# Performance work log

Hardware: AMD Instinct MI355X
Metric: run time of the kernel (lower is better)

## Reference

```python
import jax, jax.numpy as jnp
import numpy as np

B, T, D, H, L, W = 32, 512, 256, 8, 2, 10
NQ = 10000
HD = D // H


def setup_inputs():
    key = jax.random.key(0)
    ks = jax.random.split(key, 16)
    def n(k, shape, s=0.02):
        return jax.random.normal(k, shape, jnp.float32) * s
    return {
        "q": jax.random.randint(ks[0], (B, T), 0, NQ),
        "s": jax.random.randint(ks[1], (B, T), 0, 2),
        "q_embed": n(ks[2], (NQ + 1, D)),
        "s_embed": n(ks[3], (2, D)),
        "pos_embed": n(ks[4], (512, D)),
        "fusion_w": n(ks[5], (2 * D, D)),
        "fusion_b": jnp.zeros((D,), jnp.float32),
        "in_proj_w": n(ks[6], (L, D, 3 * D)),
        "in_proj_b": jnp.zeros((L, 3 * D), jnp.float32),
        "out_proj_w": n(ks[7], (L, D, D)),
        "out_proj_b": jnp.zeros((L, D), jnp.float32),
        "ln1_g": jnp.ones((L, D), jnp.float32),
        "ln1_b": jnp.zeros((L, D), jnp.float32),
        "ln2_g": jnp.ones((L, D), jnp.float32),
        "ln2_b": jnp.zeros((L, D), jnp.float32),
        "ff1_w": n(ks[8], (L, D, 4 * D)),
        "ff1_b": jnp.zeros((L, 4 * D), jnp.float32),
        "ff2_w": n(ks[9], (L, 4 * D, D)),
        "ff2_b": jnp.zeros((L, D), jnp.float32),
        "sw1": n(ks[10], (6, 32), 0.1),
        "sb1": jnp.zeros((32,), jnp.float32),
        "sw2": n(ks[11], (32, D // 4), 0.1),
        "sb2": jnp.zeros((D // 4,), jnp.float32),
        "cw1": n(ks[12], (D + D // 4, D)),
        "cb1": jnp.zeros((D,), jnp.float32),
        "cw2": n(ks[13], (D, 1)),
        "cb2": jnp.zeros((1,), jnp.float32),
    }


def _ln(x, g, b):
    mu = jnp.mean(x, -1, keepdims=True)
    var = jnp.mean(jnp.square(x - mu), -1, keepdims=True)
    return (x - mu) * jax.lax.rsqrt(var + 1e-5) * g + b


def _sliding_sum(x, w):
    # sum over trailing window of size w ending at each t, via prefix sums
    c = jnp.concatenate([jnp.zeros((x.shape[0], 1), x.dtype), jnp.cumsum(x, axis=1)], axis=1)
    t = jnp.arange(x.shape[1])
    return c[:, t + 1] - c[:, jnp.maximum(t + 1 - w, 0)]


def _stats(s, mask):
    # vectorized version of _extract_statistics (prefix-sum sliding windows)
    mf = mask.astype(jnp.float32)
    sf = s.astype(jnp.float32) * mf
    valid = _sliding_sum(mf, W)
    correct_rate = _sliding_sum(sf, W) / (valid + 1e-6)
    rc = _sliding_sum(mf, 5)
    recent_correct = _sliding_sum(sf, 5) / (rc + 1e-6)
    trans = ((s[:, 1:] != s[:, :-1]) & mask[:, 1:] & mask[:, :-1]).astype(jnp.float32)
    diff = jnp.concatenate([jnp.zeros((s.shape[0], 1), jnp.float32), trans], axis=1)
    change_rate = _sliding_sum(diff, W - 1) / (valid + 1e-6)
    # max consecutive equal run within each trailing window of size W
    sp = jnp.pad(s, ((0, 0), (W - 1, 0)))
    mp = jnp.pad(mask, ((0, 0), (W - 1, 0)))
    win_s = [sp[:, j:j + T] for j in range(W)]
    win_m = [mp[:, j:j + T] for j in range(W)]
    run = win_m[0].astype(jnp.float32)
    mx = run
    for j in range(1, W):  # fixed small window, not a data-dim loop
        eq = (win_s[j] == win_s[j - 1]) & win_m[j - 1]
        run = win_m[j].astype(jnp.float32) * (jnp.where(eq, run, 0.0) + 1.0)
        mx = jnp.maximum(mx, run)
    rel = jnp.broadcast_to(jnp.arange(T, dtype=jnp.float32) / max(T, 100), s.shape)
    cov = valid / W
    return jnp.stack([correct_rate, recent_correct, change_rate, mx / W, rel, cov], axis=-1)


def reference(q, s, q_embed, s_embed, pos_embed, fusion_w, fusion_b, in_proj_w, in_proj_b,
              out_proj_w, out_proj_b, ln1_g, ln1_b, ln2_g, ln2_b, ff1_w, ff1_b, ff2_w, ff2_b,
              sw1, sb1, sw2, sb2, cw1, cb1, cw2, cb2):
    mask = s >= 0
    qm = jnp.where(mask, q, 0)
    sm = jnp.where(mask, s, 0)
    h = jnp.concatenate([q_embed[qm], s_embed[sm]], axis=-1)  # [B,T,2D]
    h = jax.nn.relu(h @ fusion_w + fusion_b) + pos_embed[:T][None]
    causal = jnp.tril(jnp.ones((T, T), bool))
    allowed = causal[None, None] & mask[:, None, None, :]
    scale = 1.0 / (HD ** 0.5)
    for l in range(L):
        qkv = h @ in_proj_w[l] + in_proj_b[l]
        qh, kh, vh = jnp.split(qkv, 3, axis=-1)
        qh = qh.reshape(B, T, H, HD).transpose(0, 2, 1, 3)
        kh = kh.reshape(B, T, H, HD).transpose(0, 2, 1, 3)
        vh = vh.reshape(B, T, H, HD).transpose(0, 2, 1, 3)
        scores = jnp.einsum('bhqd,bhkd->bhqk', qh, kh) * scale
        scores = jnp.where(allowed, scores, -1e9)
        attn = jax.nn.softmax(scores, axis=-1)
        o = jnp.einsum('bhqk,bhkd->bhqd', attn, vh).transpose(0, 2, 1, 3).reshape(B, T, D)
        h = _ln(h + (o @ out_proj_w[l] + out_proj_b[l]), ln1_g[l], ln1_b[l])
        ff = jax.nn.gelu(h @ ff1_w[l] + ff1_b[l], approximate=False) @ ff2_w[l] + ff2_b[l]
        h = _ln(h + ff, ln2_g[l], ln2_b[l])
    sfeat = _stats(sm, mask)  # [B,T,6]
    semb = jax.nn.relu(sfeat @ sw1 + sb1) @ sw2 + sb2  # [B,T,D//4]
    comb = jnp.concatenate([h, semb], axis=-1)
    logits = (jax.nn.relu(comb @ cw1 + cb1) @ cw2 + cb2)[..., 0]
    return jnp.where(mask, logits, -1e9)
```

## Files before the change

kernel.cpp:

```cpp
#include <hip/hip_runtime.h>
#include <hip/hip_bf16.h>
#include <cmath>


using short8 = __attribute__((ext_vector_type(8))) short;
using short4v = __attribute__((ext_vector_type(4))) short;
using f32x4  = __attribute__((ext_vector_type(4))) float;

__device__ inline float gelu_f(float x) {
    return 0.5f * x * (1.0f + erff(x * 0.70710678118654752f));
}

__device__ inline short f2bf(float x) {
    union { float f; unsigned u; } v; v.f = x;
    return (short)((v.u + 0x7fffu + ((v.u >> 16) & 1u)) >> 16);
}

__device__ inline float bf2f(short v) {
    union { unsigned u; float f; } x; x.u = ((unsigned)(unsigned short)v) << 16;
    return x.f;
}

__device__ inline unsigned packbf(float lo, float hi) {
    union { float f; unsigned u; } a, b; a.f = lo; b.f = hi;
    unsigned ra = (a.u + 0x7fffu + ((a.u >> 16) & 1u)) >> 16;
    unsigned rb = (b.u + 0x7fffu + ((b.u >> 16) & 1u)) >> 16;
    return (rb << 16) | (ra & 0xffffu);
}

#define GLOAD16(gp, lp) __builtin_amdgcn_global_load_lds( \
    (const __attribute__((address_space(1))) void*)(gp), \
    (__attribute__((address_space(3))) void*)(lp), 16, 0, 0)

__global__ __launch_bounds__(256) void prep_kernel(
    const float* __restrict__ fusion_w, const float* __restrict__ in_proj_w,
    const float* __restrict__ out_proj_w, const float* __restrict__ ff1_w,
    const float* __restrict__ ff2_w, const float* __restrict__ cw1,
    short* __restrict__ wts,
    const int* __restrict__ q, const int* __restrict__ s,
    const float* __restrict__ qe, const float* __restrict__ se,
    short* __restrict__ A)
{
    __shared__ float tile[32][33];
    if (blockIdx.x < 1744) {
        const int b0[10]      = {0,128,320,512,576,640,896,1152,1408,1664};
        const int Ks[10]      = {512,256,256,256,256,256,256,1024,1024,320};
        const int Ns[10]      = {256,768,768,256,256,1024,1024,256,256,256};
        const int sidx[10]    = {0,1,1,2,2,3,3,4,4,5};
        const size_t soff[10] = {0,0,196608,0,65536,0,262144,0,262144,0};
        const size_t doff[10] = {0,131072,327680,524288,589824,655360,917504,1179648,1441792,1703936};
        const float* srcs[6] = {fusion_w, in_proj_w, out_proj_w, ff1_w, ff2_w, cw1};
        int bid = blockIdx.x;
        int mi = 0;
        while (mi < 9 && bid >= b0[mi + 1]) ++mi;
        int bl = bid - b0[mi];
        int K = Ks[mi], N = Ns[mi];
        int tx = bl % (N >> 5), ty = bl / (N >> 5);
        const float* src = srcs[sidx[mi]] + soff[mi];
        short* dst = wts + doff[mi];
        int c = threadIdx.x & 31, r = threadIdx.x >> 5;
#pragma unroll
        for (int i = 0; i < 4; ++i)
            tile[r + i * 8][c] = src[(size_t)(ty * 32 + r + i * 8) * N + tx * 32 + c];
        __syncthreads();
#pragma unroll
        for (int i = 0; i < 4; ++i)
            dst[(size_t)(tx * 32 + r + i * 8) * K + ty * 32 + c] = f2bf(tile[c][r + i * 8]);
    } else {
        int e8 = (blockIdx.x - 1744) * 256 + threadIdx.x;
        int row = e8 >> 6;
        int k8 = (e8 & 63) << 3;
        int sv = s[row];
        bool mk = sv >= 0;
        const float* src = (k8 < 256) ? qe + (size_t)(mk ? q[row] : 0) * 256 + k8
                                      : se + (size_t)(mk ? sv : 0) * 256 + (k8 - 256);
        float4 v0 = *(const float4*)src;
        float4 v1 = *(const float4*)(src + 4);
        short8 o;
        o[0] = f2bf(v0.x); o[1] = f2bf(v0.y); o[2] = f2bf(v0.z); o[3] = f2bf(v0.w);
        o[4] = f2bf(v1.x); o[5] = f2bf(v1.y); o[6] = f2bf(v1.z); o[7] = f2bf(v1.w);
        *(short8*)(A + (size_t)row * 512 + k8) = o;
    }
}

template<int EPI, int BN, int K>
__global__ __launch_bounds__(512) void gemm_bstat(
    const short* __restrict__ A, const short* __restrict__ Wt,
    const float* __restrict__ bias, short* __restrict__ out0,
    short* __restrict__ ok, short* __restrict__ ov,
    const float* __restrict__ pos)
{
    constexpr int SPR = K / 8;
    constexpr int NSTEP = K / 32;
    constexpr int NJ = BN / 16;
    __shared__ short Bs[BN * K];
    const int tid = threadIdx.x, lane = tid & 63, wv = tid >> 6;
    const int lg = lane >> 4, lr = lane & 15;
    const int n0 = blockIdx.y * BN;
    const int row0 = blockIdx.x * 128 + wv * 16;

#pragma unroll
    for (int i = 0; i < (BN * K) / 4096; ++i) {
        int slot = i * 512 + tid;
        int n = slot / SPR, posn = slot % SPR;
        int g = posn ^ (n & 7);
        GLOAD16(Wt + (size_t)(n0 + n) * K + g * 8, &Bs[slot * 8]);
    }
    const short* arow = A + (size_t)(row0 + lr) * K;
    short8 af[NSTEP];
#pragma unroll
    for (int kk = 0; kk < NSTEP; ++kk)
        af[kk] = *(const short8*)(arow + kk * 32 + lg * 8);
    __syncthreads();

    f32x4 acc[NJ] = {};
#pragma unroll
    for (int kk = 0; kk < NSTEP; ++kk) {
#pragma unroll
        for (int j = 0; j < NJ; ++j) {
            int n = j * 16 + lr;
            short8 b = *(const short8*)&Bs[n * K + (((kk * 4 + lg) ^ (n & 7)) << 3)];
            acc[j] = __builtin_amdgcn_mfma_f32_16x16x32_bf16(af[kk], b, acc[j], 0, 0, 0);
        }
    }

    if constexpr (EPI == 0) {
#pragma unroll
        for (int j = 0; j < NJ; ++j)
#pragma unroll
        for (int r = 0; r < 4; ++r) {
            int row = row0 + lg * 4 + r;
            int col = n0 + j * 16 + lr;
            float x = acc[j][r] + bias[col];
            x = fmaxf(x, 0.f) + pos[(size_t)(row & 511) * 256 + col];
            out0[(size_t)row * 256 + col] = f2bf(x);
        }
    } else if constexpr (EPI == 1) {
#pragma unroll
        for (int j = 0; j < NJ; ++j)
#pragma unroll
        for (int r = 0; r < 4; ++r) {
            int row = row0 + lg * 4 + r;
            int gcol = n0 + j * 16 + lr;
            int t = row & 511, bg = row >> 9;
            int sec = gcol >> 8, cc = gcol & 255;
            int h = cc >> 5, d = cc & 31, bh = bg * 8 + h;
            short v = f2bf(acc[j][r] + bias[gcol]);
            if (sec == 0)      out0[((size_t)bh * 512 + t) * 32 + d] = v;
            else if (sec == 1) ok[((size_t)bh * 512 + t) * 32 + d] = v;
            else {
                int kl = t & 31;
                ov[(size_t)bh * 16384 + (size_t)(t >> 5) * 1024 +
                   (size_t)((kl >> 2) & 3) * 256 + d * 8 + (((kl & 3) << 1) | ((kl >> 4) & 1))] = v;
            }
        }
    } else {
#pragma unroll
        for (int j = 0; j < NJ; ++j)
#pragma unroll
        for (int r = 0; r < 4; ++r) {
            int row = row0 + lg * 4 + r;
            int gcol = n0 + j * 16 + lr;
            float x = acc[j][r] + bias[gcol];
            out0[(size_t)row * 1024 + gcol] = f2bf(gelu_f(x));
        }
    }
}

template<int EPI>
__global__ __launch_bounds__(512) void gemm_red(
    const short* __restrict__ A, const short* __restrict__ A2,
    const short* __restrict__ Wt, const float* __restrict__ bias,
    short* __restrict__ hb,
    const float* __restrict__ gamma, const float* __restrict__ beta,
    const float* __restrict__ cw2, const float* __restrict__ cb2,
    const int* __restrict__ smask, float* __restrict__ outlog, int K)
{
    const int tid = threadIdx.x, lane = tid & 63, wv = tid >> 6;
    const int lg = lane >> 4, lr = lane & 15;
    const int wr = wv >> 2, wc = wv & 3;
    const int m0 = blockIdx.x * 64;

    __shared__ short As[2][2048];
    __shared__ short Bs[2][8192];
    __shared__ float redS[64][4];
    __shared__ float redQ[64][4];

    f32x4 acc[2][4] = {};
    const int nsteps = K >> 5;

    auto stage = [&](int buf, int step) {
        int k0 = step << 5;
        if (tid < 256) {
            int k = k0 + wv * 8;
            const short* srcA;
            if constexpr (EPI == 4)
                srcA = (k < 256) ? A + (size_t)(m0 + lane) * 256 + k
                                 : A2 + (size_t)(m0 + lane) * 64 + (k - 256);
            else
                srcA = A + (size_t)(m0 + lane) * K + k;
            GLOAD16(srcA, &As[buf][(wv * 64) * 8]);
        }
        {
            GLOAD16(Wt + (size_t)(tid & 255) * K + k0 + (tid >> 8) * 8,
                    &Bs[buf][(wv * 64) * 8]);
        }
        {
            int slot = tid + 512;
            GLOAD16(Wt + (size_t)(slot & 255) * K + k0 + (slot >> 8) * 8,
                    &Bs[buf][((wv + 8) * 64) * 8]);
        }
    };

    stage(0, 0);
    __syncthreads();
    for (int step = 0; step < nsteps; ++step) {
        int cur = step & 1;
        if (step + 1 < nsteps) stage(cur ^ 1, step + 1);
        short8 a[2], b[4];
#pragma unroll
        for (int i = 0; i < 2; ++i)
            a[i] = *(const short8*)&As[cur][(lg * 64 + wr * 32 + i * 16 + lr) * 8];
#pragma unroll
        for (int j = 0; j < 4; ++j)
            b[j] = *(const short8*)&Bs[cur][(lg * 256 + wc * 64 + j * 16 + lr) * 8];
#pragma unroll
        for (int i = 0; i < 2; ++i)
#pragma unroll
            for (int j = 0; j < 4; ++j)
                acc[i][j] = __builtin_amdgcn_mfma_f32_16x16x32_bf16(a[i], b[j], acc[i][j], 0, 0, 0);
        __syncthreads();
    }

    if constexpr (EPI == 3) {
        float ps[2][4], pq[2][4];
#pragma unroll
        for (int i = 0; i < 2; ++i)
#pragma unroll
        for (int r = 0; r < 4; ++r) { ps[i][r] = 0.f; pq[i][r] = 0.f; }
#pragma unroll
        for (int i = 0; i < 2; ++i)
#pragma unroll
        for (int j = 0; j < 4; ++j)
#pragma unroll
        for (int r = 0; r < 4; ++r) {
            int row = m0 + wr * 32 + i * 16 + lg * 4 + r;
            int col = wc * 64 + j * 16 + lr;
            float x = acc[i][j][r] + bias[col] + bf2f(hb[(size_t)row * 256 + col]);
            acc[i][j][r] = x;
            ps[i][r] += x; pq[i][r] += x * x;
        }
#pragma unroll
        for (int off = 1; off < 16; off <<= 1)
#pragma unroll
            for (int i = 0; i < 2; ++i)
#pragma unroll
            for (int r = 0; r < 4; ++r) {
                ps[i][r] += __shfl_xor(ps[i][r], off);
                pq[i][r] += __shfl_xor(pq[i][r], off);
            }
        if (lr == 0) {
#pragma unroll
            for (int i = 0; i < 2; ++i)
#pragma unroll
            for (int r = 0; r < 4; ++r) {
                int rl = wr * 32 + i * 16 + lg * 4 + r;
                redS[rl][wc] = ps[i][r]; redQ[rl][wc] = pq[i][r];
            }
        }
        __syncthreads();
#pragma unroll
        for (int i = 0; i < 2; ++i)
#pragma unroll
        for (int r = 0; r < 4; ++r) {
            int rl = wr * 32 + i * 16 + lg * 4 + r;
            int row = m0 + rl;
            float sm = redS[rl][0] + redS[rl][1] + redS[rl][2] + redS[rl][3];
            float sq = redQ[rl][0] + redQ[rl][1] + redQ[rl][2] + redQ[rl][3];
            float mu = sm * (1.f / 256.f);
            float var = sq * (1.f / 256.f) - mu * mu;
            float rstd = rsqrtf(var + 1e-5f);
#pragma unroll
            for (int j = 0; j < 4; ++j) {
                int col = wc * 64 + j * 16 + lr;
                float yv = (acc[i][j][r] - mu) * rstd * gamma[col] + beta[col];
                hb[(size_t)row * 256 + col] = f2bf(yv);
            }
        }
    } else {
        float pa[2][4];
#pragma unroll
        for (int i = 0; i < 2; ++i)
#pragma unroll
        for (int r = 0; r < 4; ++r) pa[i][r] = 0.f;
#pragma unroll
        for (int i = 0; i < 2; ++i)
#pragma unroll
        for (int j = 0; j < 4; ++j)
#pragma unroll
        for (int r = 0; r < 4; ++r) {
            int col = wc * 64 + j * 16 + lr;
            float x = fmaxf(acc[i][j][r] + bias[col], 0.f);
            pa[i][r] += x * cw2[col];
        }
#pragma unroll
        for (int off = 1; off < 16; off <<= 1)
#pragma unroll
            for (int i = 0; i < 2; ++i)
#pragma unroll
            for (int r = 0; r < 4; ++r) pa[i][r] += __shfl_xor(pa[i][r], off);
        if (lr == 0) {
#pragma unroll
            for (int i = 0; i < 2; ++i)
#pragma unroll
            for (int r = 0; r < 4; ++r)
                redS[wr * 32 + i * 16 + lg * 4 + r][wc] = pa[i][r];
        }
        __syncthreads();
        if (tid < 64) {
            int row = m0 + tid;
            float v = redS[tid][0] + redS[tid][1] + redS[tid][2] + redS[tid][3] + cb2[0];
            outlog[row] = (smask[row] >= 0) ? v : -1e9f;
        }
    }
}

__global__ __launch_bounds__(256) void attn_mfma(
    const short* __restrict__ Qg, const short* __restrict__ Kg,
    const short* __restrict__ VTg, short* __restrict__ O)
{
    __shared__ unsigned Wp[4][16][20];
    const int bh = blockIdx.x >> 2, part = blockIdx.x & 3;
    const int b = bh >> 3, h = bh & 7;
    const int wv = threadIdx.x >> 6, lane = threadIdx.x & 63;
    const int lg = lane >> 4, lr = lane & 15;
    const int slot = part * 4 + wv;
    const short* Qbh = Qg + (size_t)bh * 16384;
    const short* Kbh = Kg + (size_t)bh * 16384;
    const short* Vbh = VTg + (size_t)bh * 16384;
    const float scale = 0.17677669529663687f;

    for (int half = 0; half < 2; ++half) {
        const int tile = half ? (31 - slot) : slot;
        const int q0 = tile << 4;
        short8 qa = *(const short8*)(Qbh + (size_t)(q0 + lr) * 32 + lg * 8);
        f32x4 o0 = {}, o1 = {};
        float l_[4] = {0.f, 0.f, 0.f, 0.f};
        const int nfull = q0 >> 5;

        for (int c = 0; c <= nfull; ++c) {
            int kc = c << 5;
            short8 kf0 = *(const short8*)(Kbh + (size_t)(kc + lr) * 32 + lg * 8);
            short8 kf1 = *(const short8*)(Kbh + (size_t)(kc + 16 + lr) * 32 + lg * 8);
            f32x4 s0 = {}, s1 = {};
            s0 = __builtin_amdgcn_mfma_f32_16x16x32_bf16(qa, kf0, s0, 0, 0, 0);
            s1 = __builtin_amdgcn_mfma_f32_16x16x32_bf16(qa, kf1, s1, 0, 0, 0);
            float p0[4], p1[4];
            if (c < nfull) {
#pragma unroll
                for (int r = 0; r < 4; ++r) {
                    p0[r] = __expf(s0[r] * scale);
                    p1[r] = __expf(s1[r] * scale);
                }
            } else {
#pragma unroll
                for (int r = 0; r < 4; ++r) {
                    int qq = q0 + lg * 4 + r;
                    p0[r] = (kc + lr)      > qq ? 0.f : __expf(s0[r] * scale);
                    p1[r] = (kc + 16 + lr) > qq ? 0.f : __expf(s1[r] * scale);
                }
            }
#pragma unroll
            for (int r = 0; r < 4; ++r) {
                l_[r] += p0[r] + p1[r];
                Wp[wv][lg * 4 + r][lr] = packbf(p0[r], p1[r]);
            }
            short8 pa = *(const short8*)&Wp[wv][lr][lg * 4];
            short8 vf0 = *(const short8*)(Vbh + (size_t)c * 1024 + lg * 256 + lr * 8);
            short8 vf1 = *(const short8*)(Vbh + (size_t)c * 1024 + lg * 256 + (lr + 16) * 8);
            o0 = __builtin_amdgcn_mfma_f32_16x16x32_bf16(pa, vf0, o0, 0, 0, 0);
            o1 = __builtin_amdgcn_mfma_f32_16x16x32_bf16(pa, vf1, o1, 0, 0, 0);
        }
#pragma unroll
        for (int off = 1; off < 16; off <<= 1)
#pragma unroll
            for (int r = 0; r < 4; ++r) l_[r] += __shfl_xor(l_[r], off);
#pragma unroll
        for (int r = 0; r < 4; ++r) {
            float inv = 1.f / l_[r];
            size_t ro = ((size_t)b * 512 + q0 + lg * 4 + r) * 256 + h * 32;
            O[ro + lr] = f2bf(o0[r] * inv);
            O[ro + 16 + lr] = f2bf(o1[r] * inv);
        }
    }
}

__global__ __launch_bounds__(512) void stats_kernel(
    const int* __restrict__ s, short* __restrict__ semb,
    const float* __restrict__ sw1, const float* __restrict__ sb1,
    const float* __restrict__ sw2, const float* __restrict__ sb2)
{
    __shared__ float sv_sh[512];
    __shared__ float m_sh[512];
    __shared__ float sw2_sh[2048];
    const int b = blockIdx.x;
    const int t = threadIdx.x;
    {
        int sval = s[b * 512 + t];
        bool mk = sval >= 0;
        sv_sh[t] = mk ? (float)sval : 0.f;
        m_sh[t] = mk ? 1.f : 0.f;
    }
    for (int i = t; i < 2048; i += 512) sw2_sh[i] = sw2[i];
    __syncthreads();

    float mf10 = 0, sf10 = 0, mf5 = 0, sf5 = 0, d9 = 0;
#pragma unroll
    for (int k = 0; k < 10; ++k) {
        int idx = t - k;
        if (idx >= 0) {
            float mv = m_sh[idx], sv = sv_sh[idx];
            mf10 += mv; sf10 += sv;
            if (k < 5) { mf5 += mv; sf5 += sv; }
            if (k < 9 && idx >= 1) {
                if (sv != sv_sh[idx - 1] && mv > 0.5f && m_sh[idx - 1] > 0.5f) d9 += 1.f;
            }
        }
    }
    float run, mx;
    {
        int x0 = t - 9;
        run = (x0 >= 0) ? m_sh[x0] : 0.f;
        mx = run;
#pragma unroll
        for (int j = 1; j < 10; ++j) {
            int xc = t + j - 9, xp = xc - 1;
            float sc = (xc >= 0) ? sv_sh[xc] : 0.f;
            float sp = (xp >= 0) ? sv_sh[xp] : 0.f;
            float mc = (xc >= 0) ? m_sh[xc] : 0.f;
            float mp = (xp >= 0) ? m_sh[xp] : 0.f;
            bool eq = (sc == sp) && (mp > 0.5f);
            run = (mc > 0.5f) ? ((eq ? run : 0.f) + 1.f) : 0.f;
            mx = fmaxf(mx, run);
        }
    }
    float f[6];
    f[0] = sf10 / (mf10 + 1e-6f);
    f[1] = sf5 / (mf5 + 1e-6f);
    f[2] = d9 / (mf10 + 1e-6f);
    f[3] = mx * 0.1f;
    f[4] = (float)t * (1.f / 512.f);
    f[5] = mf10 * 0.1f;

    float hid[32];
#pragma unroll
    for (int j2 = 0; j2 < 32; ++j2) {
        float a = sb1[j2];
#pragma unroll
        for (int i = 0; i < 6; ++i) a = fmaf(f[i], sw1[i * 32 + j2], a);
        hid[j2] = fmaxf(a, 0.f);
    }
    short* orow = semb + ((size_t)b * 512 + t) * 64;
    for (int c = 0; c < 64; c += 4) {
        float v0 = sb2[c], v1 = sb2[c + 1], v2 = sb2[c + 2], v3 = sb2[c + 3];
#pragma unroll
        for (int j2 = 0; j2 < 32; ++j2) {
            float hh = hid[j2];
            v0 = fmaf(hh, sw2_sh[j2 * 64 + c], v0);
            v1 = fmaf(hh, sw2_sh[j2 * 64 + c + 1], v1);
            v2 = fmaf(hh, sw2_sh[j2 * 64 + c + 2], v2);
            v3 = fmaf(hh, sw2_sh[j2 * 64 + c + 3], v3);
        }
        short4v o; o[0] = f2bf(v0); o[1] = f2bf(v1); o[2] = f2bf(v2); o[3] = f2bf(v3);
        *(short4v*)(orow + c) = o;
    }
}

extern "C" void kernel_launch(void* const* d_in, const int* in_sizes, int n_in,
                              void* d_out, int out_size, void* d_ws, size_t ws_size,
                              hipStream_t stream) {
    const int*   q         = (const int*)d_in[0];
    const int*   s         = (const int*)d_in[1];
    const float* q_embed   = (const float*)d_in[2];
    const float* s_embed   = (const float*)d_in[3];
    const float* pos_embed = (const float*)d_in[4];
    const float* fusion_w  = (const float*)d_in[5];
    const float* fusion_b  = (const float*)d_in[6];
    const float* in_proj_w = (const float*)d_in[7];
    const float* in_proj_b = (const float*)d_in[8];
    const float* out_proj_w= (const float*)d_in[9];
    const float* out_proj_b= (const float*)d_in[10];
    const float* ln1_g     = (const float*)d_in[11];
    const float* ln1_b     = (const float*)d_in[12];
    const float* ln2_g     = (const float*)d_in[13];
    const float* ln2_b     = (const float*)d_in[14];
    const float* ff1_w     = (const float*)d_in[15];
    const float* ff1_b     = (const float*)d_in[16];
    const float* ff2_w     = (const float*)d_in[17];
    const float* ff2_b     = (const float*)d_in[18];
    const float* sw1       = (const float*)d_in[19];
    const float* sb1       = (const float*)d_in[20];
    const float* sw2       = (const float*)d_in[21];
    const float* sb2       = (const float*)d_in[22];
    const float* cw1       = (const float*)d_in[23];
    const float* cb1       = (const float*)d_in[24];
    const float* cw2       = (const float*)d_in[25];
    const float* cb2       = (const float*)d_in[26];
    float* out = (float*)d_out;

    char* base = (char*)d_ws;
    short* hb   = (short*)(base);
    short* bufA = (short*)(base + 8388608);
    short* att  = (short*)(base + 41943040);
    short* Qg   = (short*)(base + 50331648);
    short* Kg   = (short*)(base + 58720256);
    short* VTg  = (short*)(base + 67108864);
    short* semb = (short*)(base + 75497472);
    short* wts  = (short*)(base + 77594624);

    const size_t W_FUSION = 0, W_INPROJ0 = 131072, W_INPROJ1 = 327680;
    const size_t W_OUTPROJ0 = 524288, W_OUTPROJ1 = 589824;
    const size_t W_FF1_0 = 655360, W_FF1_1 = 917504;
    const size_t W_FF2_0 = 1179648, W_FF2_1 = 1441792;
    const size_t W_CW1 = 1703936;

    prep_kernel<<<5840, 256, 0, stream>>>(fusion_w, in_proj_w, out_proj_w,
                                          ff1_w, ff2_w, cw1, wts,
                                          q, s, q_embed, s_embed, bufA);
    gemm_bstat<0, 64, 512><<<dim3(128, 4), 512, 0, stream>>>(bufA,
        wts + W_FUSION, fusion_b, hb, nullptr, nullptr, pos_embed);
    for (int l = 0; l < 2; ++l) {
        gemm_bstat<1, 128, 256><<<dim3(128, 6), 512, 0, stream>>>(hb,
            wts + (l ? W_INPROJ1 : W_INPROJ0), in_proj_b + l * 768,
            Qg, Kg, VTg, nullptr);
        attn_mfma<<<1024, 256, 0, stream>>>(Qg, Kg, VTg, att);
        gemm_red<3><<<256, 512, 0, stream>>>(att, nullptr,
            wts + (l ? W_OUTPROJ1 : W_OUTPROJ0), out_proj_b + l * 256,
            hb, ln1_g + l * 256, ln1_b + l * 256,
            nullptr, nullptr, nullptr, nullptr, 256);
        gemm_bstat<2, 128, 256><<<dim3(128, 8), 512, 0, stream>>>(hb,
            wts + (l ? W_FF1_1 : W_FF1_0), ff1_b + l * 1024,
            bufA, nullptr, nullptr, nullptr);
        gemm_red<3><<<256, 512, 0, stream>>>(bufA, nullptr,
            wts + (l ? W_FF2_1 : W_FF2_0), ff2_b + l * 256,
            hb, ln2_g + l * 256, ln2_b + l * 256,
            nullptr, nullptr, nullptr, nullptr, 1024);
    }
    stats_kernel<<<32, 512, 0, stream>>>(s, semb, sw1, sb1, sw2, sb2);
    gemm_red<4><<<256, 512, 0, stream>>>(hb, semb,
        wts + W_CW1, cb1, nullptr, nullptr, nullptr,
        cw2, cb2, s, out, 320);
}
```

Baseline: 281.4 us.

## Fold stats into prep, add register-tiled out-proj/classifier GEMMs without LDS staging

Moves the per-sequence statistics MLP into extra blocks of the prep kernel, which removes one launch and lets that work overlap weight conversion. Replaces the LDS double-buffered reduction GEMM with new kernels for out-proj+LN and for the classifier head. These hold whole A rows in registers, read B straight from global/L2, and reduce LayerNorm within a wave without shared-memory syncs. FF2+LN keeps the staged path. The trade-off is higher register pressure and uncoalesced, unstaged B reads that rely on cache hits.

```diff
diff --git a/kernel.cpp b/kernel.cpp
--- a/kernel.cpp
+++ b/kernel.cpp
@@ -32,16 +32,23 @@
     (const __attribute__((address_space(1))) void*)(gp), \
     (__attribute__((address_space(3))) void*)(lp), 16, 0, 0)
 
-__global__ __launch_bounds__(256) void prep_kernel(
+__global__ __launch_bounds__(256) void prep(
     const float* __restrict__ fusion_w, const float* __restrict__ in_proj_w,
     const float* __restrict__ out_proj_w, const float* __restrict__ ff1_w,
     const float* __restrict__ ff2_w, const float* __restrict__ cw1,
     short* __restrict__ wts,
     const int* __restrict__ q, const int* __restrict__ s,
     const float* __restrict__ qe, const float* __restrict__ se,
-    short* __restrict__ A)
+    short* __restrict__ A,
+    short* __restrict__ semb,
+    const float* __restrict__ sw1, const float* __restrict__ sb1,
+    const float* __restrict__ sw2, const float* __restrict__ sb2)
 {
     __shared__ float tile[32][33];
+    __shared__ float sv_sh[512];
+    __shared__ float m_sh[512];
+    __shared__ float sw2_sh[2048];
+
     if (blockIdx.x < 1744) {
         const int b0[10]      = {0,128,320,512,576,640,896,1152,1408,1664};
         const int Ks[10]      = {512,256,256,256,256,256,256,1024,1024,320};
@@ -66,7 +73,7 @@
 #pragma unroll
         for (int i = 0; i < 4; ++i)
             dst[(size_t)(tx * 32 + r + i * 8) * K + ty * 32 + c] = f2bf(tile[c][r + i * 8]);
-    } else {
+    } else if (blockIdx.x < 5840) {
         int e8 = (blockIdx.x - 1744) * 256 + threadIdx.x;
         int row = e8 >> 6;
         int k8 = (e8 & 63) << 3;
@@ -80,11 +87,85 @@
         o[0] = f2bf(v0.x); o[1] = f2bf(v0.y); o[2] = f2bf(v0.z); o[3] = f2bf(v0.w);
         o[4] = f2bf(v1.x); o[5] = f2bf(v1.y); o[6] = f2bf(v1.z); o[7] = f2bf(v1.w);
         *(short8*)(A + (size_t)row * 512 + k8) = o;
+    } else {
+        const int b = blockIdx.x - 5840;
+        const int tt = threadIdx.x;
+        for (int t = tt; t < 512; t += 256) {
+            int sval = s[b * 512 + t];
+            bool mk = sval >= 0;
+            sv_sh[t] = mk ? (float)sval : 0.f;
+            m_sh[t] = mk ? 1.f : 0.f;
+        }
+        for (int i = tt; i < 2048; i += 256) sw2_sh[i] = sw2[i];
+        __syncthreads();
+        for (int half = 0; half < 2; ++half) {
+            const int t = tt + half * 256;
+            float mf10 = 0, sf10 = 0, mf5 = 0, sf5 = 0, d9 = 0;
+#pragma unroll
+            for (int k = 0; k < 10; ++k) {
+                int idx = t - k;
+                if (idx >= 0) {
+                    float mv = m_sh[idx], sv = sv_sh[idx];
+                    mf10 += mv; sf10 += sv;
+                    if (k < 5) { mf5 += mv; sf5 += sv; }
+                    if (k < 9 && idx >= 1) {
+                        if (sv != sv_sh[idx - 1] && mv > 0.5f && m_sh[idx - 1] > 0.5f) d9 += 1.f;
+                    }
+                }
+            }
+            float run, mx;
+            {
+                int x0 = t - 9;
+                run = (x0 >= 0) ? m_sh[x0] : 0.f;
+                mx = run;
+#pragma unroll
+                for (int j = 1; j < 10; ++j) {
+                    int xc = t + j - 9, xp = xc - 1;
+                    float sc = (xc >= 0) ? sv_sh[xc] : 0.f;
+                    float sp = (xp >= 0) ? sv_sh[xp] : 0.f;
+                    float mc = (xc >= 0) ? m_sh[xc] : 0.f;
+                    float mp = (xp >= 0) ? m_sh[xp] : 0.f;
+                    bool eq = (sc == sp) && (mp > 0.5f);
+                    run = (mc > 0.5f) ? ((eq ? run : 0.f) + 1.f) : 0.f;
+                    mx = fmaxf(mx, run);
+                }
+            }
+            float f[6];
+            f[0] = sf10 / (mf10 + 1e-6f);
+            f[1] = sf5 / (mf5 + 1e-6f);
+            f[2] = d9 / (mf10 + 1e-6f);
+            f[3] = mx * 0.1f;
+            f[4] = (float)t * (1.f / 512.f);
+            f[5] = mf10 * 0.1f;
+
+            float hid[32];
+#pragma unroll
+            for (int j2 = 0; j2 < 32; ++j2) {
+                float a = sb1[j2];
+#pragma unroll
+                for (int i = 0; i < 6; ++i) a = fmaf(f[i], sw1[i * 32 + j2], a);
+                hid[j2] = fmaxf(a, 0.f);
+            }
+            short* orow = semb + ((size_t)b * 512 + t) * 64;
+            for (int c = 0; c < 64; c += 4) {
+                float v0 = sb2[c], v1 = sb2[c + 1], v2 = sb2[c + 2], v3 = sb2[c + 3];
+#pragma unroll
+                for (int j2 = 0; j2 < 32; ++j2) {
+                    float hh = hid[j2];
+                    v0 = fmaf(hh, sw2_sh[j2 * 64 + c], v0);
+                    v1 = fmaf(hh, sw2_sh[j2 * 64 + c + 1], v1);
+                    v2 = fmaf(hh, sw2_sh[j2 * 64 + c + 2], v2);
+                    v3 = fmaf(hh, sw2_sh[j2 * 64 + c + 3], v3);
+                }
+                short4v o; o[0] = f2bf(v0); o[1] = f2bf(v1); o[2] = f2bf(v2); o[3] = f2bf(v3);
+                *(short4v*)(orow + c) = o;
+            }
+        }
     }
 }
 
 template<int EPI, int BN, int K>
-__global__ __launch_bounds__(512) void gemm_bstat(
+__device__ __forceinline__ void bstat_core(
     const short* __restrict__ A, const short* __restrict__ Wt,
     const float* __restrict__ bias, short* __restrict__ out0,
     short* __restrict__ ok, short* __restrict__ ov,
@@ -167,14 +248,122 @@
     }
 }
 
-template<int EPI>
-__global__ __launch_bounds__(512) void gemm_red(
+__global__ __launch_bounds__(512) void k_fusion(
+    const short* __restrict__ A, const short* __restrict__ Wt,
+    const float* __restrict__ bias, short* __restrict__ out0,
+    const float* __restrict__ pos)
+{ bstat_core<0, 64, 512>(A, Wt, bias, out0, nullptr, nullptr, pos); }
+
+__global__ __launch_bounds__(512) void k_qkv(
+    const short* __restrict__ A, const short* __restrict__ Wt,
+    const float* __restrict__ bias, short* __restrict__ oq,
+    short* __restrict__ ok, short* __restrict__ ov)
+{ bstat_core<1, 128, 256>(A, Wt, bias, oq, ok, ov, nullptr); }
+
+__global__ __launch_bounds__(512) void k_ff1(
+    const short* __restrict__ A, const short* __restrict__ Wt,
+    const float* __restrict__ bias, short* __restrict__ out0)
+{ bstat_core<2, 128, 256>(A, Wt, bias, out0, nullptr, nullptr, nullptr); }
+
+__global__ __launch_bounds__(256) void k_outln(
+    const short* __restrict__ A, const short* __restrict__ Wt,
+    const float* __restrict__ bias, short* __restrict__ hb,
+    const float* __restrict__ gamma, const float* __restrict__ beta)
+{
+    const int lane = threadIdx.x & 63, wv = threadIdx.x >> 6;
+    const int lg = lane >> 4, lr = lane & 15;
+    const int row0 = blockIdx.x * 64 + wv * 16;
+
+    const short* arow = A + (size_t)(row0 + lr) * 256 + lg * 8;
+    short8 af[8];
+#pragma unroll
+    for (int kk = 0; kk < 8; ++kk) af[kk] = *(const short8*)(arow + kk * 32);
+
+    f32x4 acc[16] = {};
+#pragma unroll
+    for (int kk = 0; kk < 8; ++kk)
+#pragma unroll
+    for (int j = 0; j < 16; ++j) {
+        short8 b = *(const short8*)(Wt + (size_t)(j * 16 + lr) * 256 + kk * 32 + lg * 8);
+        acc[j] = __builtin_amdgcn_mfma_f32_16x16x32_bf16(af[kk], b, acc[j], 0, 0, 0);
+    }
+
+#pragma unroll
+    for (int r = 0; r < 4; ++r) {
+        int row = row0 + lg * 4 + r;
+        float x[16], ps = 0.f, pq = 0.f;
+#pragma unroll
+        for (int j = 0; j < 16; ++j) {
+            int col = j * 16 + lr;
+            float v = acc[j][r] + bias[col] + bf2f(hb[(size_t)row * 256 + col]);
+            x[j] = v; ps += v; pq += v * v;
+        }
+#pragma unroll
+        for (int off = 1; off < 16; off <<= 1) {
+            ps += __shfl_xor(ps, off);
+            pq += __shfl_xor(pq, off);
+        }
+        float mu = ps * (1.f / 256.f);
+        float var = pq * (1.f / 256.f) - mu * mu;
+        float rstd = rsqrtf(var + 1e-5f);
+#pragma unroll
+        for (int j = 0; j < 16; ++j) {
+            int col = j * 16 + lr;
+            hb[(size_t)row * 256 + col] = f2bf((x[j] - mu) * rstd * gamma[col] + beta[col]);
+        }
+    }
+}
+
+__global__ __launch_bounds__(256) void k_clf(
     const short* __restrict__ A, const short* __restrict__ A2,
     const short* __restrict__ Wt, const float* __restrict__ bias,
-    short* __restrict__ hb,
-    const float* __restrict__ gamma, const float* __restrict__ beta,
     const float* __restrict__ cw2, const float* __restrict__ cb2,
-    const int* __restrict__ smask, float* __restrict__ outlog, int K)
+    const int* __restrict__ smask, float* __restrict__ outlog)
+{
+    const int lane = threadIdx.x & 63, wv = threadIdx.x >> 6;
+    const int lg = lane >> 4, lr = lane & 15;
+    const int row0 = blockIdx.x * 64 + wv * 16;
+
+    short8 af[10];
+    {
+        const short* arow = A + (size_t)(row0 + lr) * 256 + lg * 8;
+#pragma unroll
+        for (int kk = 0; kk < 8; ++kk) af[kk] = *(const short8*)(arow + kk * 32);
+        const short* arow2 = A2 + (size_t)(row0 + lr) * 64 + lg * 8;
+        af[8] = *(const short8*)(arow2);
+        af[9] = *(const short8*)(arow2 + 32);
+    }
+
+    f32x4 acc[16] = {};
+#pragma unroll
+    for (int kk = 0; kk < 10; ++kk)
+#pragma unroll
+    for (int j = 0; j < 16; ++j) {
+        short8 b = *(const short8*)(Wt + (size_t)(j * 16 + lr) * 320 + kk * 32 + lg * 8);
+        acc[j] = __builtin_amdgcn_mfma_f32_16x16x32_bf16(af[kk], b, acc[j], 0, 0, 0);
+    }
+
+#pragma unroll
+    for (int r = 0; r < 4; ++r) {
+        int row = row0 + lg * 4 + r;
+        float p = 0.f;
+#pragma unroll
+        for (int j = 0; j < 16; ++j) {
+            int col = j * 16 + lr;
+            float v = fmaxf(acc[j][r] + bias[col], 0.f);
+            p += v * cw2[col];
+        }
+#pragma unroll
+        for (int off = 1; off < 16; off <<= 1) p += __shfl_xor(p, off);
+        if (lr == 0)
+            outlog[row] = (smask[row] >= 0) ? p + cb2[0] : -1e9f;
+    }
+}
+
+__global__ __launch_bounds__(512) void k_ff2ln(
+    const short* __restrict__ A, const short* __restrict__ Wt,
+    const float* __restrict__ bias, short* __restrict__ hb,
+    const float* __restrict__ gamma, const float* __restrict__ beta, int K)
 {
     const int tid = threadIdx.x, lane = tid & 63, wv = tid >> 6;
     const int lg = lane >> 4, lr = lane & 15;
@@ -192,19 +381,9 @@
     auto stage = [&](int buf, int step) {
         int k0 = step << 5;
         if (tid < 256) {
-            int k = k0 + wv * 8;
-            const short* srcA;
-            if constexpr (EPI == 4)
-                srcA = (k < 256) ? A + (size_t)(m0 + lane) * 256 + k
-                                 : A2 + (size_t)(m0 + lane) * 64 + (k - 256);
-            else
-                srcA = A + (size_t)(m0 + lane) * K + k;
-            GLOAD16(srcA, &As[buf][(wv * 64) * 8]);
-        }
-        {
-            GLOAD16(Wt + (size_t)(tid & 255) * K + k0 + (tid >> 8) * 8,
-                    &Bs[buf][(wv * 64) * 8]);
-        }
+            GLOAD16(A + (size_t)(m0 + lane) * K + k0 + wv * 8, &As[buf][(wv * 64) * 8]);
+        }
+        GLOAD16(Wt + (size_t)(tid & 255) * K + k0 + (tid >> 8) * 8, &Bs[buf][(wv * 64) * 8]);
         {
             int slot = tid + 512;
             GLOAD16(Wt + (size_t)(slot & 255) * K + k0 + (slot >> 8) * 8,
@@ -232,95 +411,58 @@
         __syncthreads();
     }
 
-    if constexpr (EPI == 3) {
-        float ps[2][4], pq[2][4];
+    float ps[2][4], pq[2][4];
+#pragma unroll
+    for (int i = 0; i < 2; ++i)
+#pragma unroll
+    for (int r = 0; r < 4; ++r) { ps[i][r] = 0.f; pq[i][r] = 0.f; }
+#pragma unroll
+    for (int i = 0; i < 2; ++i)
+#pragma unroll
+    for (int j = 0; j < 4; ++j)
+#pragma unroll
+    for (int r = 0; r < 4; ++r) {
+        int row = m0 + wr * 32 + i * 16 + lg * 4 + r;
+        int col = wc * 64 + j * 16 + lr;
+        float x = acc[i][j][r] + bias[col] + bf2f(hb[(size_t)row * 256 + col]);
+        acc[i][j][r] = x;
+        ps[i][r] += x; pq[i][r] += x * x;
+    }
+#pragma unroll
+    for (int off = 1; off < 16; off <<= 1)
 #pragma unroll
         for (int i = 0; i < 2; ++i)
 #pragma unroll
-        for (int r = 0; r < 4; ++r) { ps[i][r] = 0.f; pq[i][r] = 0.f; }
-#pragma unroll
-        for (int i = 0; i < 2; ++i)
-#pragma unroll
-        for (int j = 0; j < 4; ++j)
-#pragma unroll
         for (int r = 0; r < 4; ++r) {
-            int row = m0 + wr * 32 + i * 16 + lg * 4 + r;
-            int col = wc * 64 + j * 16 + lr;
-            float x = acc[i][j][r] + bias[col] + bf2f(hb[(size_t)row * 256 + col]);
-            acc[i][j][r] = x;
-            ps[i][r] += x; pq[i][r] += x * x;
-        }
-#pragma unroll
-        for (int off = 1; off < 16; off <<= 1)
-#pragma unroll
-            for (int i = 0; i < 2; ++i)
-#pragma unroll
-            for (int r = 0; r < 4; ++r) {
-                ps[i][r] += __shfl_xor(ps[i][r], off);
-                pq[i][r] += __shfl_xor(pq[i][r], off);
-            }
-        if (lr == 0) {
-#pragma unroll
-            for (int i = 0; i < 2; ++i)
-#pragma unroll
-            for (int r = 0; r < 4; ++r) {
-                int rl = wr * 32 + i * 16 + lg * 4 + r;
-                redS[rl][wc] = ps[i][r]; redQ[rl][wc] = pq[i][r];
-            }
-        }
-        __syncthreads();
+            ps[i][r] += __shfl_xor(ps[i][r], off);
+            pq[i][r] += __shfl_xor(pq[i][r], off);
+        }
+    if (lr == 0) {
 #pragma unroll
         for (int i = 0; i < 2; ++i)
 #pragma unroll
         for (int r = 0; r < 4; ++r) {
             int rl = wr * 32 + i * 16 + lg * 4 + r;
-            int row = m0 + rl;
-            float sm = redS[rl][0] + redS[rl][1] + redS[rl][2] + redS[rl][3];
-            float sq = redQ[rl][0] + redQ[rl][1] + redQ[rl][2] + redQ[rl][3];
-            float mu = sm * (1.f / 256.f);
-            float var = sq * (1.f / 256.f) - mu * mu;
-            float rstd = rsqrtf(var + 1e-5f);
-#pragma unroll
-            for (int j = 0; j < 4; ++j) {
-                int col = wc * 64 + j * 16 + lr;
-                float yv = (acc[i][j][r] - mu) * rstd * gamma[col] + beta[col];
-                hb[(size_t)row * 256 + col] = f2bf(yv);
-            }
-        }
-    } else {
-        float pa[2][4];
-#pragma unroll
-        for (int i = 0; i < 2; ++i)
-#pragma unroll
-        for (int r = 0; r < 4; ++r) pa[i][r] = 0.f;
-#pragma unroll
-        for (int i = 0; i < 2; ++i)
-#pragma unroll
-        for (int j = 0; j < 4; ++j)
-#pragma unroll
-        for (int r = 0; r < 4; ++r) {
+            redS[rl][wc] = ps[i][r]; redQ[rl][wc] = pq[i][r];
+        }
+    }
+    __syncthreads();
+#pragma unroll
+    for (int i = 0; i < 2; ++i)
+#pragma unroll
+    for (int r = 0; r < 4; ++r) {
+        int rl = wr * 32 + i * 16 + lg * 4 + r;
+        int row = m0 + rl;
+        float sm = redS[rl][0] + redS[rl][1] + redS[rl][2] + redS[rl][3];
+        float sq = redQ[rl][0] + redQ[rl][1] + redQ[rl][2] + redQ[rl][3];
+        float mu = sm * (1.f / 256.f);
+        float var = sq * (1.f / 256.f) - mu * mu;
+        float rstd = rsqrtf(var + 1e-5f);
+#pragma unroll
+        for (int j = 0; j < 4; ++j) {
             int col = wc * 64 + j * 16 + lr;
-            float x = fmaxf(acc[i][j][r] + bias[col], 0.f);
-            pa[i][r] += x * cw2[col];
-        }
-#pragma unroll
-        for (int off = 1; off < 16; off <<= 1)
-#pragma unroll
-            for (int i = 0; i < 2; ++i)
-#pragma unroll
-            for (int r = 0; r < 4; ++r) pa[i][r] += __shfl_xor(pa[i][r], off);
-        if (lr == 0) {
-#pragma unroll
-            for (int i = 0; i < 2; ++i)
-#pragma unroll
-            for (int r = 0; r < 4; ++r)
-                redS[wr * 32 + i * 16 + lg * 4 + r][wc] = pa[i][r];
-        }
-        __syncthreads();
-        if (tid < 64) {
-            int row = m0 + tid;
-            float v = redS[tid][0] + redS[tid][1] + redS[tid][2] + redS[tid][3] + cb2[0];
-            outlog[row] = (smask[row] >= 0) ? v : -1e9f;
+            float yv = (acc[i][j][r] - mu) * rstd * gamma[col] + beta[col];
+            hb[(size_t)row * 256 + col] = f2bf(yv);
         }
     }
 }
@@ -392,87 +534,6 @@
             O[ro + lr] = f2bf(o0[r] * inv);
             O[ro + 16 + lr] = f2bf(o1[r] * inv);
         }
-    }
-}
-
-__global__ __launch_bounds__(512) void stats_kernel(
-    const int* __restrict__ s, short* __restrict__ semb,
-    const float* __restrict__ sw1, const float* __restrict__ sb1,
-    const float* __restrict__ sw2, const float* __restrict__ sb2)
-{
-    __shared__ float sv_sh[512];
-    __shared__ float m_sh[512];
-    __shared__ float sw2_sh[2048];
-    const int b = blockIdx.x;
-    const int t = threadIdx.x;
-    {
-        int sval = s[b * 512 + t];
-        bool mk = sval >= 0;
-        sv_sh[t] = mk ? (float)sval : 0.f;
-        m_sh[t] = mk ? 1.f : 0.f;
-    }
-    for (int i = t; i < 2048; i += 512) sw2_sh[i] = sw2[i];
-    __syncthreads();
-
-    float mf10 = 0, sf10 = 0, mf5 = 0, sf5 = 0, d9 = 0;
-#pragma unroll
-    for (int k = 0; k < 10; ++k) {
-        int idx = t - k;
-        if (idx >= 0) {
-            float mv = m_sh[idx], sv = sv_sh[idx];
-            mf10 += mv; sf10 += sv;
-            if (k < 5) { mf5 += mv; sf5 += sv; }
-            if (k < 9 && idx >= 1) {
-                if (sv != sv_sh[idx - 1] && mv > 0.5f && m_sh[idx - 1] > 0.5f) d9 += 1.f;
-            }
-        }
-    }
-    float run, mx;
-    {
-        int x0 = t - 9;
-        run = (x0 >= 0) ? m_sh[x0] : 0.f;
-        mx = run;
-#pragma unroll
-        for (int j = 1; j < 10; ++j) {
-            int xc = t + j - 9, xp = xc - 1;
-            float sc = (xc >= 0) ? sv_sh[xc] : 0.f;
-            float sp = (xp >= 0) ? sv_sh[xp] : 0.f;
-            float mc = (xc >= 0) ? m_sh[xc] : 0.f;
-            float mp = (xp >= 0) ? m_sh[xp] : 0.f;
-            bool eq = (sc == sp) && (mp > 0.5f);
-            run = (mc > 0.5f) ? ((eq ? run : 0.f) + 1.f) : 0.f;
-            mx = fmaxf(mx, run);
-        }
-    }
-    float f[6];
-    f[0] = sf10 / (mf10 + 1e-6f);
-    f[1] = sf5 / (mf5 + 1e-6f);
-    f[2] = d9 / (mf10 + 1e-6f);
-    f[3] = mx * 0.1f;
-    f[4] = (float)t * (1.f / 512.f);
-    f[5] = mf10 * 0.1f;
-
-    float hid[32];
-#pragma unroll
-    for (int j2 = 0; j2 < 32; ++j2) {
-        float a = sb1[j2];
-#pragma unroll
-        for (int i = 0; i < 6; ++i) a = fmaf(f[i], sw1[i * 32 + j2], a);
-        hid[j2] = fmaxf(a, 0.f);
-    }
-    short* orow = semb + ((size_t)b * 512 + t) * 64;
-    for (int c = 0; c < 64; c += 4) {
-        float v0 = sb2[c], v1 = sb2[c + 1], v2 = sb2[c + 2], v3 = sb2[c + 3];
-#pragma unroll
-        for (int j2 = 0; j2 < 32; ++j2) {
-            float hh = hid[j2];
-            v0 = fmaf(hh, sw2_sh[j2 * 64 + c], v0);
-            v1 = fmaf(hh, sw2_sh[j2 * 64 + c + 1], v1);
-            v2 = fmaf(hh, sw2_sh[j2 * 64 + c + 2], v2);
-            v3 = fmaf(hh, sw2_sh[j2 * 64 + c + 3], v3);
-        }
-        short4v o; o[0] = f2bf(v0); o[1] = f2bf(v1); o[2] = f2bf(v2); o[3] = f2bf(v3);
-        *(short4v*)(orow + c) = o;
     }
 }
 
@@ -524,30 +585,25 @@
     const size_t W_FF2_0 = 1179648, W_FF2_1 = 1441792;
     const size_t W_CW1 = 1703936;
 
-    prep_kernel<<<5840, 256, 0, stream>>>(fusion_w, in_proj_w, out_proj_w,
-                                          ff1_w, ff2_w, cw1, wts,
-                                          q, s, q_embed, s_embed, bufA);
-    gemm_bstat<0, 64, 512><<<dim3(128, 4), 512, 0, stream>>>(bufA,
-        wts + W_FUSION, fusion_b, hb, nullptr, nullptr, pos_embed);
+    prep<<<5872, 256, 0, stream>>>(fusion_w, in_proj_w, out_proj_w,
+                                   ff1_w, ff2_w, cw1, wts,
+                                   q, s, q_embed, s_embed, bufA,
+                                   semb, sw1, sb1, sw2, sb2);
+    k_fusion<<<dim3(128, 4), 512, 0, stream>>>(bufA, wts + W_FUSION, fusion_b,
+                                               hb, pos_embed);
     for (int l = 0; l < 2; ++l) {
-        gemm_bstat<1, 128, 256><<<dim3(128, 6), 512, 0, stream>>>(hb,
-            wts + (l ? W_INPROJ1 : W_INPROJ0), in_proj_b + l * 768,
-            Qg, Kg, VTg, nullptr);
+        k_qkv<<<dim3(128, 6), 512, 0, stream>>>(hb,
+            wts + (l ? W_INPROJ1 : W_INPROJ0), in_proj_b + l * 768, Qg, Kg, VTg);
         attn_mfma<<<1024, 256, 0, stream>>>(Qg, Kg, VTg, att);
-        gemm_red<3><<<256, 512, 0, stream>>>(att, nullptr,
+        k_outln<<<256, 256, 0, stream>>>(att,
             wts + (l ? W_OUTPROJ1 : W_OUTPROJ0), out_proj_b + l * 256,
-            hb, ln1_g + l * 256, ln1_b + l * 256,
-            nullptr, nullptr, nullptr, nullptr, 256);
-        gemm_bstat<2, 128, 256><<<dim3(128, 8), 512, 0, stream>>>(hb,
-            wts + (l ? W_FF1_1 : W_FF1_0), ff1_b + l * 1024,
-            bufA, nullptr, nullptr, nullptr);
-        gemm_red<3><<<256, 512, 0, stream>>>(bufA, nullptr,
+            hb, ln1_g + l * 256, ln1_b + l * 256);
+        k_ff1<<<dim3(128, 8), 512, 0, stream>>>(hb,
+            wts + (l ? W_FF1_1 : W_FF1_0), ff1_b + l * 1024, bufA);
+        k_ff2ln<<<256, 512, 0, stream>>>(bufA,
             wts + (l ? W_FF2_1 : W_FF2_0), ff2_b + l * 256,
-            hb, ln2_g + l * 256, ln2_b + l * 256,
-            nullptr, nullptr, nullptr, nullptr, 1024);
-    }
-    stats_kernel<<<32, 512, 0, stream>>>(s, semb, sw1, sb1, sw2, sb2);
-    gemm_red<4><<<256, 512, 0, stream>>>(hb, semb,
-        wts + W_CW1, cb1, nullptr, nullptr, nullptr,
-        cw2, cb2, s, out, 320);
-}
+            hb, ln2_g + l * 256, ln2_b + l * 256, 1024);
+    }
+    k_clf<<<256, 256, 0, stream>>>(hb, semb, wts + W_CW1, cb1,
+                                   cw2, cb2, s, out);
+}
```

Result: slower. 334.0 us (+18.7%).
